# Kernel tuning notes

Measured on AMD Instinct MI355X. Metric: run time of the kernel, lower is better.

Reference implementation:

```python
import jax, jax.numpy as jnp
import numpy as np

DIM = 256
HEADS = 8
PERCENT = 0.25


def setup_inputs() -> dict:
    key = jax.random.key(0)
    k1, k2, k3 = jax.random.split(key, 3)
    B, N, C = 8, 1024, DIM
    X = jax.random.normal(k1, (B, N, C), jnp.float32)
    adj = jax.random.uniform(k2, (B, N, N), jnp.float32)
    adj = 0.5 * (adj + adj.transpose(0, 2, 1))  # symmetric dense adjacency
    mask = jnp.ones((B, N), jnp.float32)
    # qkv weight of Att_scores: Linear(dim, 2*dim, bias=False)
    Wqkv = jax.random.normal(k3, (C, 2 * C), jnp.float32) * (1.0 / np.sqrt(C))
    return {"X": X, "adj": adj, "mask": mask, "Wqkv": Wqkv}


def reference(X, adj, mask, Wqkv):
    B, N, C = X.shape
    H = HEADS
    scale = (C // H) ** (-0.5)
    # Att_scores: qkv -> q,k per head; scores[b,i] = sum_h sum_j (q_h[i] . k_h[j]) * scale
    # Since heads partition C, this collapses to q[i] . (sum_j k[j]) without an NxN matrix.
    qkv = jnp.einsum('bnc,cd->bnd', X, Wqkv)  # [B,N,2C]
    q, k = qkv[..., :C], qkv[..., C:]
    ksum = k.sum(axis=1)  # [B,C]
    scores = scale * jnp.einsum('bnc,bc->bn', q, ksum)  # [B,N]
    NEG = jnp.float32(-1e9)
    scores = jnp.where(mask > 0, scores, NEG)
    # top-k node selection: k_max = ceil(percent * N), per-graph k_i = ceil(percent * n_i)
    k_max = int(np.ceil(PERCENT * N))
    vals, idx = jax.lax.top_k(scores, k_max)  # [B,k_max]
    k_i = jnp.ceil(PERCENT * mask.sum(axis=1)).astype(jnp.int32)  # [B]
    new_mask = (jnp.arange(k_max)[None, :] < k_i[:, None]).astype(X.dtype)  # [B,k_max]
    gate = jnp.tanh(vals) * new_mask  # score gating keeps grads flowing to selection
    # gather selected node features and the induced sub-adjacency
    new_X = jnp.take_along_axis(X, idx[:, :, None], axis=1) * gate[..., None]  # [B,k_max,C]
    rows = jnp.take_along_axis(adj, idx[:, :, None], axis=1)          # [B,k_max,N]
    new_adj = jnp.take_along_axis(rows, idx[:, None, :], axis=2)      # [B,k_max,k_max]
    new_adj = new_adj * new_mask[:, :, None] * new_mask[:, None, :]
    return new_X, new_adj, new_mask
```

## Files before the change

### kernel.cpp

```cpp
#include <hip/hip_runtime.h>

#define BB 8
#define NN 1024
#define CC 256
#define KMAX 256
#define NGRP 32
#define SCALE 0.17677669529663687f
#define NEGV -1000000000.0f

__device__ __forceinline__ unsigned long long shfl_xor_u64(unsigned long long v, int m) {
    unsigned lo = (unsigned)v, hi = (unsigned)(v >> 32);
    lo = (unsigned)__shfl_xor((int)lo, m, 64);
    hi = (unsigned)__shfl_xor((int)hi, m, 64);
    return (((unsigned long long)hi) << 32) | lo;
}

__global__ void k_xsum(const float* __restrict__ X, float* __restrict__ partial) {
    int b = blockIdx.x, g = blockIdx.y, c = threadIdx.x;
    const float* p = X + ((size_t)b * NN + (size_t)g * (NN / NGRP)) * CC + c;
    float acc = 0.f;
#pragma unroll 8
    for (int r = 0; r < NN / NGRP; ++r) acc += p[(size_t)r * CC];
    partial[((size_t)b * NGRP + g) * CC + c] = acc;
}

__global__ void k_v(const float* __restrict__ partial, const float* __restrict__ W,
                    float* __restrict__ v) {
    int b = blockIdx.x, t = threadIdx.x;
    __shared__ float xs[CC];
    __shared__ float ks[CC];
    float acc0 = 0.f;
    const float* pp = partial + (size_t)b * NGRP * CC + t;
#pragma unroll
    for (int g = 0; g < NGRP; ++g) acc0 += pp[(size_t)g * CC];
    xs[t] = acc0;
    __syncthreads();
    float acc = 0.f;
    const float* Wk = W + CC + t;
#pragma unroll 8
    for (int cp = 0; cp < CC; ++cp) acc += xs[cp] * Wk[(size_t)cp * (2 * CC)];
    ks[t] = acc;
    __syncthreads();
    const float4* Wq4 = (const float4*)(W + (size_t)t * (2 * CC));
    const float4* ks4 = (const float4*)ks;
    float acc2 = 0.f;
#pragma unroll 8
    for (int c4 = 0; c4 < CC / 4; ++c4) {
        float4 w = Wq4[c4], k4 = ks4[c4];
        acc2 += w.x * k4.x + w.y * k4.y + w.z * k4.z + w.w * k4.w;
    }
    v[b * CC + t] = acc2;
}

__global__ void k_scores(const float* __restrict__ X, const float* __restrict__ mask,
                         const float* __restrict__ v, float* __restrict__ scores) {
    int b = blockIdx.x, t = threadIdx.x;
    int wave = t >> 6, lane = t & 63;
    int n = blockIdx.y * 4 + wave;
    const float4* vv = (const float4*)(v + b * CC);
    float4 v4 = vv[lane];
    const float4* row = (const float4*)(X + ((size_t)b * NN + n) * CC);
    float4 x4 = row[lane];
    float acc = x4.x * v4.x + x4.y * v4.y + x4.z * v4.z + x4.w * v4.w;
#pragma unroll
    for (int o = 32; o > 0; o >>= 1) acc += __shfl_down(acc, o, 64);
    if (lane == 0) {
        float m = mask[b * NN + n];
        scores[b * NN + n] = (m > 0.f) ? SCALE * acc : NEGV;
    }
}

__global__ __launch_bounds__(1024) void k_topk(const float* __restrict__ scores,
                                               const float* __restrict__ mask,
                                               int* __restrict__ idx, float* __restrict__ gate,
                                               float* __restrict__ out_mask,
                                               int* __restrict__ kiws) {
    int b = blockIdx.x, t = threadIdx.x;
    int lane = t & 63;
    __shared__ unsigned long long keysL[NN];
    __shared__ float redw[16];
    __shared__ int ki_s;

    float s = scores[b * NN + t];
    unsigned u = __float_as_uint(s);
    u = (u & 0x80000000u) ? ~u : (u | 0x80000000u);
    unsigned long long key = (((unsigned long long)(~u)) << 32) | (unsigned)t;

    float m = mask[b * NN + t];
#pragma unroll
    for (int o = 32; o > 0; o >>= 1) m += __shfl_down(m, o, 64);
    if (lane == 0) redw[t >> 6] = m;

    for (int k = 2; k <= NN; k <<= 1) {
        bool up = ((t & k) == 0);
        for (int j = k >> 1; j >= 64; j >>= 1) {
            __syncthreads();
            keysL[t] = key;
            __syncthreads();
            unsigned long long p = keysL[t ^ j];
            bool lower = ((t & j) == 0);
            bool doMax = (up != lower);
            key = doMax ? (key > p ? key : p) : (key < p ? key : p);
        }
        int jstart = (k >> 1) < 64 ? (k >> 1) : 32;
        for (int j = jstart; j >= 1; j >>= 1) {
            unsigned long long p = shfl_xor_u64(key, j);
            bool lower = ((lane & j) == 0);
            bool doMax = (up != lower);
            key = doMax ? (key > p ? key : p) : (key < p ? key : p);
        }
    }
    __syncthreads();
    if (t == 0) {
        float tot = 0.f;
        for (int i = 0; i < 16; ++i) tot += redw[i];
        ki_s = (int)ceilf(0.25f * tot);
    }
    __syncthreads();

    if (t < KMAX) {
        int ki = ki_s;
        int id = (int)(key & 0xFFFFFFFFu);
        unsigned u2 = ~((unsigned)(key >> 32));
        float val = (u2 & 0x80000000u) ? __uint_as_float(u2 ^ 0x80000000u)
                                       : __uint_as_float(~u2);
        float nm = (t < ki) ? 1.f : 0.f;
        idx[b * KMAX + t] = id;
        gate[b * KMAX + t] = tanhf(val) * nm;
        out_mask[b * KMAX + t] = nm;
        if (t == 0) kiws[b] = ki;
    }
}

__global__ void k_gather(const float* __restrict__ X, const float* __restrict__ adj,
                         const int* __restrict__ idx, const float* __restrict__ gate,
                         const int* __restrict__ kiws,
                         float* __restrict__ outX, float* __restrict__ outA) {
    int i = blockIdx.x, b = blockIdx.y, t = threadIdx.x;
    __shared__ int idxL[KMAX];
    __shared__ float rowL[NN];
    idxL[t] = idx[b * KMAX + t];
    __syncthreads();
    int ki = kiws[b];
    int mi = idxL[i];
    float gi = gate[b * KMAX + i];
    float nmi = (i < ki) ? 1.f : 0.f;

    const float* xr = X + ((size_t)b * NN + mi) * CC;
    outX[((size_t)b * KMAX + i) * CC + t] = xr[t] * gi;

    const float4* ar4 = (const float4*)(adj + ((size_t)b * NN + mi) * NN);
    ((float4*)rowL)[t] = ar4[t];
    __syncthreads();
    float nmj = (t < ki) ? 1.f : 0.f;
    outA[((size_t)b * KMAX + i) * KMAX + t] = rowL[idxL[t]] * nmi * nmj;
}

extern "C" void kernel_launch(void* const* d_in, const int* in_sizes, int n_in,
                              void* d_out, int out_size, void* d_ws, size_t ws_size,
                              hipStream_t stream) {
    const float* X    = (const float*)d_in[0];
    const float* adj  = (const float*)d_in[1];
    const float* mask = (const float*)d_in[2];
    const float* W    = (const float*)d_in[3];
    float* out = (float*)d_out;

    char* ws = (char*)d_ws;
    float* partial = (float*)(ws + 0);
    float* v       = (float*)(ws + 32768);
    float* scores  = (float*)(ws + 40960);
    int*   idxp    = (int*)(ws + 73728);
    float* gate    = (float*)(ws + 81920);
    int*   kiws    = (int*)(ws + 90112);

    float* outX = out;
    float* outA = out + (size_t)BB * KMAX * CC;
    float* outM = outA + (size_t)BB * KMAX * KMAX;

    k_xsum<<<dim3(BB, NGRP), CC, 0, stream>>>(X, partial);
    k_v<<<BB, CC, 0, stream>>>(partial, W, v);
    k_scores<<<dim3(BB, NN / 4), 256, 0, stream>>>(X, mask, v, scores);
    k_topk<<<BB, NN, 0, stream>>>(scores, mask, idxp, gate, outM, kiws);
    k_gather<<<dim3(KMAX, BB), KMAX, 0, stream>>>(X, adj, idxp, gate, kiws, outX, outA);
}
```

Baseline: 120.3 us.

## Replace bitonic-sort top-k with parallel rank counting across more blocks

The single-block-per-batch bitonic sort with many block barriers is replaced by a rank-by-counting kernel. Each thread compares its score key against all 1024 scores of its batch and scatters itself to its rank if that rank falls in the top 256. This spreads the work over 32 blocks instead of 8 and removes the sort's barriers. The cost is O(N^2) comparisons, all reading the same scores through cache, and the ordering of ties is decided by an index tiebreak.

```diff
diff --git a/kernel.cpp b/kernel.cpp
--- a/kernel.cpp
+++ b/kernel.cpp
@@ -132,6 +132,54 @@
     }
 }
 
+__global__ __launch_bounds__(256) void k_rank(const float* __restrict__ scores,
+                                              const float* __restrict__ mask,
+                                              int* __restrict__ idx,
+                                              float* __restrict__ gate,
+                                              float* __restrict__ out_mask,
+                                              int* __restrict__ kiws) {
+    int b = blockIdx.y, t = threadIdx.x;
+    int n = blockIdx.x * 256 + t;
+    int lane = t & 63;
+
+    __shared__ float redw[4];
+    __shared__ int ki_s;
+    const float* mb = mask + (size_t)b * NN;
+    float m = mb[t] + mb[t + 256] + mb[t + 512] + mb[t + 768];
+#pragma unroll
+    for (int o = 32; o > 0; o >>= 1) m += __shfl_down(m, o, 64);
+    if (lane == 0) redw[t >> 6] = m;
+    __syncthreads();
+    if (t == 0) ki_s = (int)ceilf(0.25f * (redw[0] + redw[1] + redw[2] + redw[3]));
+
+    const float* sb = scores + (size_t)b * NN;
+    float sn = sb[n];
+    unsigned un = __float_as_uint(sn);
+    un = (un & 0x80000000u) ? ~un : (un | 0x80000000u);
+    unsigned long long kn =
+        (((unsigned long long)un) << 32) | (unsigned)(NN - 1 - n);
+
+    int rank = 0;
+#pragma unroll 8
+    for (int mm = 0; mm < NN; ++mm) {
+        unsigned um = __float_as_uint(sb[mm]);
+        um = (um & 0x80000000u) ? ~um : (um | 0x80000000u);
+        unsigned long long km =
+            (((unsigned long long)um) << 32) | (unsigned)(NN - 1 - mm);
+        rank += (km > kn) ? 1 : 0;
+    }
+
+    __syncthreads();
+    if (rank < KMAX) {
+        int ki = ki_s;
+        float nm = (rank < ki) ? 1.f : 0.f;
+        idx[b * KMAX + rank] = n;
+        gate[b * KMAX + rank] = tanhf(sn) * nm;
+        out_mask[b * KMAX + rank] = nm;
+    }
+    if (t == 0 && blockIdx.x == 0) kiws[b] = ki_s;
+}
+
 __global__ void k_gather(const float* __restrict__ X, const float* __restrict__ adj,
                          const int* __restrict__ idx, const float* __restrict__ gate,
                          const int* __restrict__ kiws,
@@ -180,6 +228,6 @@
     k_xsum<<<dim3(BB, NGRP), CC, 0, stream>>>(X, partial);
     k_v<<<BB, CC, 0, stream>>>(partial, W, v);
     k_scores<<<dim3(BB, NN / 4), 256, 0, stream>>>(X, mask, v, scores);
-    k_topk<<<BB, NN, 0, stream>>>(scores, mask, idxp, gate, outM, kiws);
+    k_rank<<<dim3(NN / 256, BB), 256, 0, stream>>>(scores, mask, idxp, gate, outM, kiws);
     k_gather<<<dim3(KMAX, BB), KMAX, 0, stream>>>(X, adj, idxp, gate, kiws, outX, outA);
 }
```

Result: slower. 147.9 us (+23.0%).
